# Kernel optimization log

Hardware: AMD Instinct MI355X
Metric: run time of the kernel (lower is better)

## Reference

```python
import jax, jax.numpy as jnp
import numpy as np

B, L, V, H = 64, 2048, 1024, 256
HALF = H // 2


def setup_inputs() -> dict:
    key = jax.random.key(0)
    ks = jax.random.split(key, 8)
    s = lambda k, shape, scale=0.05: jax.random.normal(k, shape, jnp.float32) * scale
    return {
        "seq": jax.random.randint(ks[0], (B, L), 0, V),
        "embed": s(ks[1], (V, H)),
        "w1": s(ks[2], (H, 2 * H)), "b1": jnp.zeros((2 * H,), jnp.float32),
        "w2": s(ks[3], (2 * H, H)), "b2": jnp.zeros((H,), jnp.float32),
        "ln_g": jnp.ones((H,), jnp.float32), "ln_b": jnp.zeros((H,), jnp.float32),
        "kp_w": s(ks[4], (H, H)), "kp_b": jnp.zeros((H,), jnp.float32),
        "out_w": s(ks[5], (H, V)), "out_b": jnp.zeros((V,), jnp.float32),
    }


def _forward(seq, embed, w1, b1, w2, b2, ln_g, ln_b, kp_w, kp_b, out_w, out_b):
    # Encoder: embed -> FFN residual -> LayerNorm
    e = embed[seq]                                    # [B, L, H]
    ff = jax.nn.relu(e @ w1 + b1) @ w2 + b2           # [B, L, H]
    x = e + ff
    mu = x.mean(-1, keepdims=True)
    var = jnp.mean((x - mu) ** 2, -1, keepdims=True)
    h = (x - mu) * jax.lax.rsqrt(var + 1e-5) * ln_g + ln_b

    # Shared key projection for all timesteps at once
    proj = h @ kp_w + kp_b                            # [B, L, H]
    ks_all = proj[:, : L - 1, :HALF]                  # [B, L-1, half]
    ke_all = proj[:, : L - 1, HALF:]                  # [B, L-1, half]
    scale = (jnp.arange(L - 1, dtype=jnp.float32) + 1.0) / L  # (t+1)/L

    def step(carry, inp):
        M_s, M_e = carry
        k_s, k_e, sc = inp                            # [B,half], [B,half], scalar
        vps = jnp.einsum('bij,bj->bi', M_s, k_s)
        dvs = k_s - vps / (jnp.sum(k_s * k_s, -1, keepdims=True) + 1e-6)
        M_s = M_s + jnp.einsum('bi,bj->bij', dvs, k_s)
        vpe = jnp.einsum('bij,bj->bi', M_e, k_e)
        dve = k_e - vpe / (jnp.sum(k_e * k_e, -1, keepdims=True) + 1e-6)
        M_e = M_e + sc * jnp.einsum('bi,bj->bij', dve, k_e)
        return (M_s, M_e), None

    M0 = jnp.zeros((B, HALF, HALF), jnp.float32)
    (M_s, M_e), _ = jax.lax.scan(
        step, (M0, M0),
        (ks_all.transpose(1, 0, 2), ke_all.transpose(1, 0, 2), scale))

    q = proj[:, -1, :]                                # query from last step
    cs = jnp.einsum('bij,bj->bi', M_s, q[:, :HALF])
    ce = jnp.einsum('bij,bj->bi', M_e, q[:, HALF:])
    return jnp.concatenate([cs, ce], -1) @ out_w + out_b  # [B, V]


def reference(seq, embed, w1, b1, w2, b2, ln_g, ln_b, kp_w, kp_b, out_w, out_b):
    return _forward(seq, embed, w1, b1, w2, b2, ln_g, ln_b, kp_w, kp_b, out_w, out_b)
```

## Files before the change

kernel.cpp:

```cpp
#include <hip/hip_runtime.h>
#include <hip/hip_bf16.h>
#include <stdint.h>

#define B_SZ 64
#define L_SZ 2048
#define V_SZ 1024
#define H_SZ 256
#define HALF_SZ 128
#define NTOK (B_SZ * L_SZ)
#define CH 16384

typedef unsigned short ushort_t;
typedef __attribute__((ext_vector_type(8))) short bf16x8;
typedef __attribute__((ext_vector_type(4))) float f32x4;

__device__ __forceinline__ ushort_t f2bf(float f) {
    __hip_bfloat16 h = __float2bfloat16(f);
    return *reinterpret_cast<ushort_t*>(&h);
}

__global__ __launch_bounds__(256) void cvt_bf16_k(
    const float* __restrict__ src, ushort_t* __restrict__ dst, int n)
{
    int i = (blockIdx.x * 256 + threadIdx.x) * 4;
    if (i >= n) return;
    float4 v = *(const float4*)(src + i);
    uint2 pk;
    pk.x = (uint32_t)f2bf(v.x) | ((uint32_t)f2bf(v.y) << 16);
    pk.y = (uint32_t)f2bf(v.z) | ((uint32_t)f2bf(v.w) << 16);
    *(uint2*)(dst + i) = pk;
}

__global__ __launch_bounds__(256) void transpose_cvt_k(
    const float* __restrict__ src, ushort_t* __restrict__ dst, int K, int N)
{
    int idx = blockIdx.x * 256 + threadIdx.x;
    if (idx >= K * N) return;
    int n = idx / K;
    int k = idx - n * K;
    dst[idx] = f2bf(src[(size_t)k * N + n]);
}

template <int MODE, int K, int N>
__global__ __launch_bounds__(256) void gemm_mfma(
    const ushort_t* __restrict__ A, const ushort_t* __restrict__ BT,
    const float* __restrict__ bias, void* __restrict__ Cp,
    const int* __restrict__ seq, const float* __restrict__ embed)
{
    __shared__ __align__(16) ushort_t Asm[128 * 64];
    __shared__ __align__(16) ushort_t Bsm[128 * 64];

    const int tid = threadIdx.x;
    const int m0 = blockIdx.x * 128;
    const int n0 = blockIdx.y * 128;
    const int w = tid >> 6;
    const int l = tid & 63;
    const int wr = w >> 1;
    const int wc = w & 1;

    const ushort_t* arow[4];
    const ushort_t* brow[4];
#pragma unroll
    for (int i = 0; i < 4; ++i) {
        const int flat = i * 256 + tid;
        const int r = flat >> 3;
        const int gr = (MODE == 1) ? seq[m0 + r] : (m0 + r);
        arow[i] = A + (size_t)gr * K;
        brow[i] = BT + (size_t)(n0 + r) * K;
    }

    f32x4 acc[4][4];
#pragma unroll
    for (int mi = 0; mi < 4; ++mi)
#pragma unroll
        for (int nj = 0; nj < 4; ++nj)
            acc[mi][nj] = (f32x4){0.f, 0.f, 0.f, 0.f};

    for (int kt = 0; kt < K / 64; ++kt) {
#pragma unroll
        for (int i = 0; i < 4; ++i) {
            const int flat = i * 256 + tid;
            const int r = flat >> 3;
            const int c = flat & 7;
            const int cs = c ^ (r & 7);
            uint4 av = *(const uint4*)(arow[i] + kt * 64 + c * 8);
            *(uint4*)&Asm[r * 64 + cs * 8] = av;
            uint4 bv = *(const uint4*)(brow[i] + kt * 64 + c * 8);
            *(uint4*)&Bsm[r * 64 + cs * 8] = bv;
        }
        __syncthreads();
#pragma unroll
        for (int kh = 0; kh < 2; ++kh) {
            bf16x8 af[4], bfr[4];
#pragma unroll
            for (int mi = 0; mi < 4; ++mi) {
                const int r = wr * 64 + mi * 16 + (l & 15);
                const int c = (kh * 4 + (l >> 4)) ^ (r & 7);
                af[mi] = *(const bf16x8*)&Asm[r * 64 + c * 8];
            }
#pragma unroll
            for (int nj = 0; nj < 4; ++nj) {
                const int r = wc * 64 + nj * 16 + (l & 15);
                const int c = (kh * 4 + (l >> 4)) ^ (r & 7);
                bfr[nj] = *(const bf16x8*)&Bsm[r * 64 + c * 8];
            }
#pragma unroll
            for (int mi = 0; mi < 4; ++mi)
#pragma unroll
                for (int nj = 0; nj < 4; ++nj)
                    acc[mi][nj] = __builtin_amdgcn_mfma_f32_16x16x32_bf16(
                        af[mi], bfr[nj], acc[mi][nj], 0, 0, 0);
        }
        __syncthreads();
    }

    const int cl = l & 15;
    const int rg = l >> 4;
    float bv[4];
#pragma unroll
    for (int nj = 0; nj < 4; ++nj)
        bv[nj] = bias[n0 + wc * 64 + nj * 16 + cl];

#pragma unroll
    for (int mi = 0; mi < 4; ++mi) {
#pragma unroll
        for (int i = 0; i < 4; ++i) {
            const int row = m0 + wr * 64 + mi * 16 + rg * 4 + i;
            const float* erow = (MODE == 2)
                ? (embed + (size_t)seq[row] * H_SZ) : nullptr;
#pragma unroll
            for (int nj = 0; nj < 4; ++nj) {
                const int gn = n0 + wc * 64 + nj * 16 + cl;
                float v = acc[mi][nj][i] + bv[nj];
                if (MODE == 1) {
                    v = fmaxf(v, 0.f);
                    ((ushort_t*)Cp)[(size_t)row * N + gn] = f2bf(v);
                } else if (MODE == 2) {
                    ((float*)Cp)[(size_t)row * N + gn] = v + erow[gn];
                } else {
                    ((float*)Cp)[(size_t)row * N + gn] = v;
                }
            }
        }
    }
}

__global__ __launch_bounds__(256) void ln_k(
    const float* __restrict__ x, const float* __restrict__ g,
    const float* __restrict__ bt, ushort_t* __restrict__ h)
{
    const int token = blockIdx.x * 4 + (threadIdx.x >> 6);
    const int lane = threadIdx.x & 63;
    const float* xr = x + (size_t)token * H_SZ + lane * 4;
    const float4 v = *(const float4*)xr;
    float s = v.x + v.y + v.z + v.w;
    float sq = v.x * v.x + v.y * v.y + v.z * v.z + v.w * v.w;
#pragma unroll
    for (int m = 1; m < 64; m <<= 1) {
        s += __shfl_xor(s, m);
        sq += __shfl_xor(sq, m);
    }
    const float mu = s * (1.f / H_SZ);
    const float var = sq * (1.f / H_SZ) - mu * mu;
    const float rs = rsqrtf(var + 1e-5f);
    const int idx = lane * 4;
    const float4 gg = *(const float4*)(g + idx);
    const float4 bb = *(const float4*)(bt + idx);
    ushort_t o0 = f2bf((v.x - mu) * rs * gg.x + bb.x);
    ushort_t o1 = f2bf((v.y - mu) * rs * gg.y + bb.y);
    ushort_t o2 = f2bf((v.z - mu) * rs * gg.z + bb.z);
    ushort_t o3 = f2bf((v.w - mu) * rs * gg.w + bb.w);
    uint2 pk;
    pk.x = (uint32_t)o0 | ((uint32_t)o1 << 16);
    pk.y = (uint32_t)o2 | ((uint32_t)o3 << 16);
    *(uint2*)(h + (size_t)token * H_SZ + idx) = pk;
}

__global__ __launch_bounds__(256) void gram8_k(
    const float* __restrict__ proj, float* __restrict__ g8)
{
    const int pair = blockIdx.y;
    const int b = pair >> 1;
    const int half = pair & 1;
    const int bi = blockIdx.x * 4 + (threadIdx.x >> 6);
    const int l = threadIdx.x & 63;

    const float* kbase = proj + (size_t)b * L_SZ * H_SZ + half * HALF_SZ;

    float2 kk[8];
#pragma unroll
    for (int i = 0; i < 8; ++i) {
        const int tok = bi * 8 + 7 - i;
        kk[i] = *(const float2*)(kbase + (size_t)tok * H_SZ + 2 * l);
    }

    float r[36];
#pragma unroll
    for (int i = 0; i < 8; ++i)
        r[i] = kk[i].x * kk[i].x + kk[i].y * kk[i].y;
#pragma unroll
    for (int i = 1; i < 8; ++i)
#pragma unroll
        for (int j = 0; j < i; ++j)
            r[8 + i * (i - 1) / 2 + j] = kk[i].x * kk[j].x + kk[i].y * kk[j].y;

#pragma unroll
    for (int m = 1; m < 64; m <<= 1)
#pragma unroll
        for (int t = 0; t < 36; ++t)
            r[t] += __shfl_xor(r[t], m);

    const float invL = 1.0f / (float)L_SZ;
    float al[8], be[8];
#pragma unroll
    for (int i = 0; i < 8; ++i) {
        const int tok = bi * 8 + 7 - i;
        const float bet = (tok == L_SZ - 1)
            ? 0.f : (half ? (float)(tok + 1) * invL : 1.0f);
        be[i] = bet;
        al[i] = bet / (r[i] + 1e-6f);
    }

    if (l == 0) {
        float* out = g8 + ((size_t)pair * 256 + bi) * 48;
#pragma unroll
        for (int i = 1; i < 8; ++i)
#pragma unroll
            for (int j = 0; j < i; ++j)
                out[i * (i - 1) / 2 + j] = al[j] * r[8 + i * (i - 1) / 2 + j];
#pragma unroll
        for (int i = 0; i < 8; ++i) {
            out[28 + i] = al[i];
            out[36 + i] = be[i];
        }
    }
}

__global__ __launch_bounds__(64) void scan_bw8_k(
    const float* __restrict__ proj, const float* __restrict__ g8,
    float* __restrict__ cbuf)
{
    const int pair = blockIdx.x;
    const int b = pair >> 1;
    const int half = pair & 1;
    const int l = threadIdx.x;

    const float* kbase = proj + (size_t)b * L_SZ * H_SZ + half * HALF_SZ;
    const float* gbase = g8 + (size_t)pair * 256 * 48;

    float2 v = *(const float2*)(kbase + (size_t)(L_SZ - 1) * H_SZ + 2 * l);
    float2 c = make_float2(0.f, 0.f);

    float2 kc[8], kn[8], kf[8];
    float Gc[48], Gf[48];

#pragma unroll
    for (int i = 0; i < 8; ++i) {
        kc[i] = *(const float2*)(kbase + (size_t)(255 * 8 + 7 - i) * H_SZ + 2 * l);
        kn[i] = *(const float2*)(kbase + (size_t)(254 * 8 + 7 - i) * H_SZ + 2 * l);
    }
    {
        const float4* gp = (const float4*)(gbase + (size_t)255 * 48);
#pragma unroll
        for (int i = 0; i < 12; ++i) *(float4*)(Gc + 4 * i) = gp[i];
    }

    for (int bi = 255; bi >= 0; --bi) {
        const int kp = (bi >= 2) ? bi - 2 : 0;
        const int gp_ = (bi >= 1) ? bi - 1 : 0;
#pragma unroll
        for (int i = 0; i < 8; ++i)
            kf[i] = *(const float2*)(kbase + (size_t)(kp * 8 + 7 - i) * H_SZ + 2 * l);
        {
            const float4* gp2 = (const float4*)(gbase + (size_t)gp_ * 48);
#pragma unroll
            for (int i = 0; i < 12; ++i) *(float4*)(Gf + 4 * i) = gp2[i];
        }

        float a[8];
#pragma unroll
        for (int i = 0; i < 8; ++i)
            a[i] = kc[i].x * v.x + kc[i].y * v.y;
#pragma unroll
        for (int m = 1; m < 64; m <<= 1)
#pragma unroll
            for (int i = 0; i < 8; ++i)
                a[i] += __shfl_xor(a[i], m);

        float d[8];
#pragma unroll
        for (int i = 0; i < 8; ++i) {
            float t = a[i];
            const int off = i * (i - 1) / 2;
#pragma unroll
            for (int j = 0; j < i; ++j)
                t -= Gc[off + j] * d[j];
            d[i] = t;
        }

        float ad[8], bd[8];
#pragma unroll
        for (int i = 0; i < 8; ++i) {
            ad[i] = Gc[28 + i] * d[i];
            bd[i] = Gc[36 + i] * d[i];
        }

#pragma unroll
        for (int i = 0; i < 8; ++i) {
            v.x = fmaf(-ad[i], kc[i].x, v.x);
            v.y = fmaf(-ad[i], kc[i].y, v.y);
            c.x = fmaf(bd[i], kc[i].x, c.x);
            c.y = fmaf(bd[i], kc[i].y, c.y);
        }

#pragma unroll
        for (int i = 0; i < 8; ++i) { kc[i] = kn[i]; kn[i] = kf[i]; }
#pragma unroll
        for (int j = 0; j < 48; ++j) Gc[j] = Gf[j];
    }

    *(float2*)(cbuf + b * H_SZ + half * HALF_SZ + 2 * l) = c;
}

__global__ __launch_bounds__(256) void out_k(
    const float* __restrict__ c, const float* __restrict__ w,
    const float* __restrict__ ob, float* __restrict__ out)
{
    const int b = blockIdx.x >> 2;
    const int v = ((blockIdx.x & 3) << 8) + threadIdx.x;
    const float* cb = c + b * H_SZ;
    float acc = ob[v];
#pragma unroll 4
    for (int hh = 0; hh < H_SZ; ++hh)
        acc = fmaf(cb[hh], w[(size_t)hh * V_SZ + v], acc);
    out[(size_t)b * V_SZ + v] = acc;
}

extern "C" void kernel_launch(void* const* d_in, const int* in_sizes, int n_in,
                              void* d_out, int out_size, void* d_ws, size_t ws_size,
                              hipStream_t stream)
{
    const int*   seq   = (const int*)d_in[0];
    const float* embed = (const float*)d_in[1];
    const float* w1    = (const float*)d_in[2];
    const float* b1    = (const float*)d_in[3];
    const float* w2    = (const float*)d_in[4];
    const float* b2    = (const float*)d_in[5];
    const float* ln_g  = (const float*)d_in[6];
    const float* ln_b  = (const float*)d_in[7];
    const float* kp_w  = (const float*)d_in[8];
    const float* kp_b  = (const float*)d_in[9];
    const float* out_w = (const float*)d_in[10];
    const float* out_b = (const float*)d_in[11];

    char* ws = (char*)d_ws;
    size_t off = 0;
    auto alloc = [&](size_t bytes) -> void* {
        void* p = ws + off;
        off += (bytes + 255) & ~(size_t)255;
        return p;
    };

    float*    proj = (float*)alloc((size_t)NTOK * H_SZ * sizeof(float));
    ushort_t* t1_c = (ushort_t*)alloc((size_t)CH * 512 * sizeof(ushort_t));
    float*    x_c  = (float*)alloc((size_t)CH * H_SZ * sizeof(float));
    ushort_t* h_c  = (ushort_t*)alloc((size_t)CH * H_SZ * sizeof(ushort_t));
    float*    g8   = (float*)alloc((size_t)128 * 256 * 48 * sizeof(float));
    float*    cbuf = (float*)alloc((size_t)B_SZ * H_SZ * sizeof(float));
    ushort_t* embed_bf = (ushort_t*)alloc((size_t)V_SZ * H_SZ * 2);
    ushort_t* w1T = (ushort_t*)alloc((size_t)512 * 256 * 2);
    ushort_t* w2T = (ushort_t*)alloc((size_t)256 * 512 * 2);
    ushort_t* kpT = (ushort_t*)alloc((size_t)256 * 256 * 2);
    float*    outp = (float*)d_out;

    const dim3 blk(256);

    cvt_bf16_k<<<dim3((V_SZ * H_SZ) / 1024), blk, 0, stream>>>(
        embed, embed_bf, V_SZ * H_SZ);
    transpose_cvt_k<<<dim3((256 * 512) / 256), blk, 0, stream>>>(w1, w1T, 256, 512);
    transpose_cvt_k<<<dim3((512 * 256) / 256), blk, 0, stream>>>(w2, w2T, 512, 256);
    transpose_cvt_k<<<dim3((256 * 256) / 256), blk, 0, stream>>>(kp_w, kpT, 256, 256);

    for (int c = 0; c < NTOK / CH; ++c) {
        const int base = c * CH;
        const int* seq_c = seq + base;
        gemm_mfma<1, 256, 512><<<dim3(CH / 128, 4), blk, 0, stream>>>(
            embed_bf, w1T, b1, t1_c, seq_c, nullptr);
        gemm_mfma<2, 512, 256><<<dim3(CH / 128, 2), blk, 0, stream>>>(
            t1_c, w2T, b2, x_c, seq_c, embed);
        ln_k<<<dim3(CH / 4), blk, 0, stream>>>(x_c, ln_g, ln_b, h_c);
        gemm_mfma<3, 256, 256><<<dim3(CH / 128, 2), blk, 0, stream>>>(
            h_c, kpT, kp_b, proj + (size_t)base * H_SZ, seq_c, nullptr);
    }

    gram8_k<<<dim3(64, 128), blk, 0, stream>>>(proj, g8);
    scan_bw8_k<<<dim3(128), dim3(64), 0, stream>>>(proj, g8, cbuf);
    out_k<<<dim3(B_SZ * 4), blk, 0, stream>>>(cbuf, out_w, out_b, outp);
}
```

Measured before the change: 911.6 us.

## Precompute inverted triangular solve in gram kernel and rotate scan buffers

The gram kernel now inverts the unit lower-triangular coefficient matrix per 8-token block, so the sequential scan computes d by a shallow, tree-structured matrix-vector product instead of forward substitution. The scan loop is unrolled three ways with rotating register buffers instead of copying prefetched keys and coefficients each iteration. Empty asm statements keep the prefetched values live so the loads are issued early. The work on the serial critical path shrinks, at the cost of extra per-block work in the parallel gram kernel, higher register pressure, and a small change in floating-point rounding order.

```diff
diff --git a/kernel.cpp b/kernel.cpp
--- a/kernel.cpp
+++ b/kernel.cpp
@@ -187,22 +187,23 @@
 
     const float* kbase = proj + (size_t)b * L_SZ * H_SZ + half * HALF_SZ;
 
-    float2 kk[8];
+    float kx[8], ky[8];
 #pragma unroll
     for (int i = 0; i < 8; ++i) {
         const int tok = bi * 8 + 7 - i;
-        kk[i] = *(const float2*)(kbase + (size_t)tok * H_SZ + 2 * l);
+        const float2 t = *(const float2*)(kbase + (size_t)tok * H_SZ + 2 * l);
+        kx[i] = t.x; ky[i] = t.y;
     }
 
     float r[36];
 #pragma unroll
     for (int i = 0; i < 8; ++i)
-        r[i] = kk[i].x * kk[i].x + kk[i].y * kk[i].y;
+        r[i] = kx[i] * kx[i] + ky[i] * ky[i];
 #pragma unroll
     for (int i = 1; i < 8; ++i)
 #pragma unroll
         for (int j = 0; j < i; ++j)
-            r[8 + i * (i - 1) / 2 + j] = kk[i].x * kk[j].x + kk[i].y * kk[j].y;
+            r[8 + i * (i - 1) / 2 + j] = kx[i] * kx[j] + ky[i] * ky[j];
 
 #pragma unroll
     for (int m = 1; m < 64; m <<= 1)
@@ -221,13 +222,28 @@
         al[i] = bet / (r[i] + 1e-6f);
     }
 
+    float Lw[28];
+#pragma unroll
+    for (int i = 1; i < 8; ++i)
+#pragma unroll
+        for (int j = 0; j < i; ++j)
+            Lw[i * (i - 1) / 2 + j] = al[j] * r[8 + i * (i - 1) / 2 + j];
+    float Wv[28];
+#pragma unroll
+    for (int j = 0; j < 7; ++j)
+#pragma unroll
+        for (int i = j + 1; i < 8; ++i) {
+            float s = Lw[i * (i - 1) / 2 + j];
+#pragma unroll
+            for (int m = j + 1; m < i; ++m)
+                s += Lw[i * (i - 1) / 2 + m] * Wv[m * (m - 1) / 2 + j];
+            Wv[i * (i - 1) / 2 + j] = -s;
+        }
+
     if (l == 0) {
         float* out = g8 + ((size_t)pair * 256 + bi) * 48;
 #pragma unroll
-        for (int i = 1; i < 8; ++i)
-#pragma unroll
-            for (int j = 0; j < i; ++j)
-                out[i * (i - 1) / 2 + j] = al[j] * r[8 + i * (i - 1) / 2 + j];
+        for (int t = 0; t < 28; ++t) out[t] = Wv[t];
 #pragma unroll
         for (int i = 0; i < 8; ++i) {
             out[28 + i] = al[i];
@@ -236,7 +252,7 @@
     }
 }
 
-__global__ __launch_bounds__(64) void scan_bw8_k(
+__global__ __launch_bounds__(64, 1) void scan_bw8_k(
     const float* __restrict__ proj, const float* __restrict__ g8,
     float* __restrict__ cbuf)
 {
@@ -248,78 +264,125 @@
     const float* kbase = proj + (size_t)b * L_SZ * H_SZ + half * HALF_SZ;
     const float* gbase = g8 + (size_t)pair * 256 * 48;
 
-    float2 v = *(const float2*)(kbase + (size_t)(L_SZ - 1) * H_SZ + 2 * l);
-    float2 c = make_float2(0.f, 0.f);
-
-    float2 kc[8], kn[8], kf[8];
-    float Gc[48], Gf[48];
-
-#pragma unroll
-    for (int i = 0; i < 8; ++i) {
-        kc[i] = *(const float2*)(kbase + (size_t)(255 * 8 + 7 - i) * H_SZ + 2 * l);
-        kn[i] = *(const float2*)(kbase + (size_t)(254 * 8 + 7 - i) * H_SZ + 2 * l);
-    }
+    float vx, vy, cx = 0.f, cy = 0.f;
     {
-        const float4* gp = (const float4*)(gbase + (size_t)255 * 48);
-#pragma unroll
-        for (int i = 0; i < 12; ++i) *(float4*)(Gc + 4 * i) = gp[i];
-    }
-
-    for (int bi = 255; bi >= 0; --bi) {
-        const int kp = (bi >= 2) ? bi - 2 : 0;
-        const int gp_ = (bi >= 1) ? bi - 1 : 0;
-#pragma unroll
-        for (int i = 0; i < 8; ++i)
-            kf[i] = *(const float2*)(kbase + (size_t)(kp * 8 + 7 - i) * H_SZ + 2 * l);
-        {
-            const float4* gp2 = (const float4*)(gbase + (size_t)gp_ * 48);
-#pragma unroll
-            for (int i = 0; i < 12; ++i) *(float4*)(Gf + 4 * i) = gp2[i];
-        }
-
-        float a[8];
-#pragma unroll
-        for (int i = 0; i < 8; ++i)
-            a[i] = kc[i].x * v.x + kc[i].y * v.y;
-#pragma unroll
-        for (int m = 1; m < 64; m <<= 1)
-#pragma unroll
-            for (int i = 0; i < 8; ++i)
-                a[i] += __shfl_xor(a[i], m);
-
-        float d[8];
-#pragma unroll
-        for (int i = 0; i < 8; ++i) {
-            float t = a[i];
-            const int off = i * (i - 1) / 2;
-#pragma unroll
-            for (int j = 0; j < i; ++j)
-                t -= Gc[off + j] * d[j];
-            d[i] = t;
-        }
-
-        float ad[8], bd[8];
-#pragma unroll
-        for (int i = 0; i < 8; ++i) {
-            ad[i] = Gc[28 + i] * d[i];
-            bd[i] = Gc[36 + i] * d[i];
-        }
-
-#pragma unroll
-        for (int i = 0; i < 8; ++i) {
-            v.x = fmaf(-ad[i], kc[i].x, v.x);
-            v.y = fmaf(-ad[i], kc[i].y, v.y);
-            c.x = fmaf(bd[i], kc[i].x, c.x);
-            c.y = fmaf(bd[i], kc[i].y, c.y);
-        }
-
-#pragma unroll
-        for (int i = 0; i < 8; ++i) { kc[i] = kn[i]; kn[i] = kf[i]; }
-#pragma unroll
-        for (int j = 0; j < 48; ++j) Gc[j] = Gf[j];
-    }
-
-    *(float2*)(cbuf + b * H_SZ + half * HALF_SZ + 2 * l) = c;
+        const float2 q = *(const float2*)(kbase + (size_t)(L_SZ - 1) * H_SZ + 2 * l);
+        vx = q.x; vy = q.y;
+    }
+
+    float kAx[8], kAy[8], kBx[8], kBy[8], kCx[8], kCy[8];
+    float gA[48], gB[48], gC[48];
+
+#define LOADK(KX, KY, blk) {                                                  \
+    const int bb_ = (blk) < 0 ? 0 : (blk);                                    \
+    const float* kb_ = kbase + (size_t)bb_ * 8 * H_SZ + 2 * l;                \
+    _Pragma("unroll")                                                         \
+    for (int i_ = 0; i_ < 8; ++i_) {                                          \
+        const float2 t_ = *(const float2*)(kb_ + (size_t)(7 - i_) * H_SZ);    \
+        KX[i_] = t_.x; KY[i_] = t_.y;                                         \
+    } }
+
+#define LOADG(GG, blk) {                                                      \
+    const int bb_ = (blk) < 0 ? 0 : (blk);                                    \
+    const float* gs_ = gbase + (size_t)bb_ * 48;                              \
+    _Pragma("unroll")                                                         \
+    for (int i_ = 0; i_ < 12; ++i_) {                                         \
+        const float4 t_ = *(const float4*)(gs_ + 4 * i_);                     \
+        GG[4*i_+0] = t_.x; GG[4*i_+1] = t_.y;                                 \
+        GG[4*i_+2] = t_.z; GG[4*i_+3] = t_.w;                                 \
+    } }
+
+#define KEEP8(A0,A1,A2,A3,A4,A5,A6,A7)                                        \
+    asm volatile("" :: "v"(A0), "v"(A1), "v"(A2), "v"(A3),                    \
+                       "v"(A4), "v"(A5), "v"(A6), "v"(A7));
+
+#define KEEPK(KX, KY)                                                         \
+    KEEP8(KX[0],KX[1],KX[2],KX[3],KX[4],KX[5],KX[6],KX[7])                    \
+    KEEP8(KY[0],KY[1],KY[2],KY[3],KY[4],KY[5],KY[6],KY[7])
+
+#define KEEPG(GG)                                                             \
+    KEEP8(GG[0],GG[1],GG[2],GG[3],GG[4],GG[5],GG[6],GG[7])                    \
+    KEEP8(GG[8],GG[9],GG[10],GG[11],GG[12],GG[13],GG[14],GG[15])              \
+    KEEP8(GG[16],GG[17],GG[18],GG[19],GG[20],GG[21],GG[22],GG[23])            \
+    KEEP8(GG[24],GG[25],GG[26],GG[27],GG[28],GG[29],GG[30],GG[31])            \
+    KEEP8(GG[32],GG[33],GG[34],GG[35],GG[36],GG[37],GG[38],GG[39])            \
+    KEEP8(GG[40],GG[41],GG[42],GG[43],GG[44],GG[45],GG[46],GG[47])
+
+#define ITER(bi_, KCX, KCY, GC, KFX, KFY, GF, DOPF) {                         \
+    if (DOPF) { LOADK(KFX, KFY, (bi_) - 2) LOADG(GF, (bi_) - 2) }             \
+    float a_[8];                                                              \
+    _Pragma("unroll")                                                         \
+    for (int i_ = 0; i_ < 8; ++i_)                                            \
+        a_[i_] = KCX[i_] * vx + KCY[i_] * vy;                                 \
+    _Pragma("unroll")                                                         \
+    for (int m_ = 1; m_ < 64; m_ <<= 1)                                       \
+        _Pragma("unroll")                                                     \
+        for (int i_ = 0; i_ < 8; ++i_)                                        \
+            a_[i_] += __shfl_xor(a_[i_], m_);                                 \
+                          \
+    float d_[8];                                                              \
+    d_[0] = a_[0];                                                            \
+    d_[1] = fmaf(GC[0], a_[0], a_[1]);                                        \
+    d_[2] = fmaf(GC[1], a_[0], a_[2]) + GC[2] * a_[1];                        \
+    d_[3] = (fmaf(GC[3], a_[0], a_[3]) + GC[4] * a_[1]) + GC[5] * a_[2];      \
+    d_[4] = (fmaf(GC[6], a_[0], a_[4]) + GC[7] * a_[1])                       \
+          + (GC[8] * a_[2] + GC[9] * a_[3]);                                  \
+    d_[5] = ((fmaf(GC[10], a_[0], a_[5]) + GC[11] * a_[1])                    \
+          + (GC[12] * a_[2] + GC[13] * a_[3])) + GC[14] * a_[4];              \
+    d_[6] = ((fmaf(GC[15], a_[0], a_[6]) + GC[16] * a_[1])                    \
+          + (GC[17] * a_[2] + GC[18] * a_[3]))                                \
+          + (GC[19] * a_[4] + GC[20] * a_[5]);                                \
+    d_[7] = ((fmaf(GC[21], a_[0], a_[7]) + GC[22] * a_[1])                    \
+          + (GC[23] * a_[2] + GC[24] * a_[3]))                                \
+          + ((GC[25] * a_[4] + GC[26] * a_[5]) + GC[27] * a_[6]);             \
+    float ad_[8], bd_[8];                                                     \
+    _Pragma("unroll")                                                         \
+    for (int i_ = 0; i_ < 8; ++i_) {                                          \
+        ad_[i_] = GC[28 + i_] * d_[i_];                                       \
+        bd_[i_] = GC[36 + i_] * d_[i_];                                       \
+    }                                                                         \
+    const float sx_ = (fmaf(ad_[0], KCX[0], ad_[1] * KCX[1])                  \
+                     + fmaf(ad_[2], KCX[2], ad_[3] * KCX[3]))                 \
+                    + (fmaf(ad_[4], KCX[4], ad_[5] * KCX[5])                  \
+                     + fmaf(ad_[6], KCX[6], ad_[7] * KCX[7]));                \
+    const float sy_ = (fmaf(ad_[0], KCY[0], ad_[1] * KCY[1])                  \
+                     + fmaf(ad_[2], KCY[2], ad_[3] * KCY[3]))                 \
+                    + (fmaf(ad_[4], KCY[4], ad_[5] * KCY[5])                  \
+                     + fmaf(ad_[6], KCY[6], ad_[7] * KCY[7]));                \
+    const float tx_ = (fmaf(bd_[0], KCX[0], bd_[1] * KCX[1])                  \
+                     + fmaf(bd_[2], KCX[2], bd_[3] * KCX[3]))                 \
+                    + (fmaf(bd_[4], KCX[4], bd_[5] * KCX[5])                  \
+                     + fmaf(bd_[6], KCX[6], bd_[7] * KCX[7]));                \
+    const float ty_ = (fmaf(bd_[0], KCY[0], bd_[1] * KCY[1])                  \
+                     + fmaf(bd_[2], KCY[2], bd_[3] * KCY[3]))                 \
+                    + (fmaf(bd_[4], KCY[4], bd_[5] * KCY[5])                  \
+                     + fmaf(bd_[6], KCY[6], bd_[7] * KCY[7]));                \
+    vx -= sx_; vy -= sy_; cx += tx_; cy += ty_;                               \
+    if (DOPF) { KEEPK(KFX, KFY) KEEPG(GF) }                                   \
+    }
+
+    LOADK(kAx, kAy, 255) LOADG(gA, 255)
+    LOADK(kBx, kBy, 254) LOADG(gB, 254)
+
+    int bi = 255;
+#pragma unroll 1
+    for (int t3 = 0; t3 < 85; ++t3) {
+        ITER(bi,     kAx, kAy, gA, kCx, kCy, gC, 1)
+        ITER(bi - 1, kBx, kBy, gB, kAx, kAy, gA, 1)
+        ITER(bi - 2, kCx, kCy, gC, kBx, kBy, gB, 1)
+        bi -= 3;
+    }
+    ITER(0, kAx, kAy, gA, kBx, kBy, gB, 0)
+
+#undef ITER
+#undef KEEPG
+#undef KEEPK
+#undef KEEP8
+#undef LOADG
+#undef LOADK
+
+    cbuf[b * H_SZ + half * HALF_SZ + 2 * l] = cx;
+    cbuf[b * H_SZ + half * HALF_SZ + 2 * l + 1] = cy;
 }
 
 __global__ __launch_bounds__(256) void out_k(
```

Result: faster. 770.0 us (-15.5%).
